# Kernel tuning notes

Hardware: AMD Instinct MI355X
Metric: run time of the kernel (lower is better)

Reference implementation:

```python
import jax, jax.numpy as jnp
import numpy as np

N = 50000   # nodes
E = 800000  # edges (avg degree 16)
D = 96      # in = hid = out
BN_EPS = 1e-5


def setup_inputs() -> dict:
    key = jax.random.key(0)
    ks = jax.random.split(key, 16)
    features = jax.random.normal(ks[0], (N, D), jnp.float32)
    src = jax.random.randint(ks[1], (E,), 0, N)
    dst = jax.random.randint(ks[2], (E,), 0, N)
    bound = 1.0 / np.sqrt(D)
    def lin(kw, kb):
        W = jax.random.uniform(kw, (D, D), jnp.float32, -bound, bound)
        b = jax.random.uniform(kb, (D,), jnp.float32, -bound, bound)
        return W, b
    W1, b1 = lin(ks[3], ks[4])
    W2, b2 = lin(ks[5], ks[6])
    W3, b3 = lin(ks[7], ks[8])
    gamma1 = jnp.ones((D,), jnp.float32)
    beta1 = jnp.zeros((D,), jnp.float32)
    gamma2 = jnp.ones((D,), jnp.float32)
    beta2 = jnp.zeros((D,), jnp.float32)
    return dict(features=features, W1=W1, b1=b1, gamma1=gamma1, beta1=beta1,
                W2=W2, b2=b2, gamma2=gamma2, beta2=beta2, W3=W3, b3=b3,
                src=src, dst=dst)


def _gin_conv(h, W, b, src, dst, inv_deg):
    # mean-aggregate incoming neighbor features, eps = 0: (h + mean_nb) @ W + b
    agg = jax.ops.segment_sum(h[src], dst, num_segments=N) * inv_deg[:, None]
    return (h + agg) @ W + b


def _batchnorm(x, gamma, beta):
    mu = jnp.mean(x, axis=0)
    var = jnp.mean((x - mu) ** 2, axis=0)  # biased, as torch BN training
    return (x - mu) * jax.lax.rsqrt(var + BN_EPS) * gamma + beta


def reference(features, W1, b1, gamma1, beta1, W2, b2, gamma2, beta2, W3, b3, src, dst):
    deg = jax.ops.segment_sum(jnp.ones((E,), jnp.float32), dst, num_segments=N)
    inv_deg = jnp.where(deg > 0, 1.0 / jnp.maximum(deg, 1.0), 0.0)
    h = _gin_conv(features, W1, b1, src, dst, inv_deg)
    h = jax.nn.relu(_batchnorm(h, gamma1, beta1))  # dropout p=0 -> identity
    h = _gin_conv(h, W2, b2, src, dst, inv_deg)
    h = jax.nn.relu(_batchnorm(h, gamma2, beta2))
    h = _gin_conv(h, W3, b3, src, dst, inv_deg)
    return h
```

## Files before the change

kernel.cpp:

```cpp
#include <hip/hip_runtime.h>

#define FD 96
#define NB12 12
#define BSH 7
#define BNODES 128
#define NBLK 256

typedef float  f32x4 __attribute__((ext_vector_type(4)));
typedef short  s16x8 __attribute__((ext_vector_type(8)));

__device__ __forceinline__ unsigned short f2bf(float x) {
    unsigned u = __float_as_uint(x);
    u = (u + 0x7fffu + ((u >> 16) & 1u)) >> 16;
    return (unsigned short)u;
}
__device__ __forceinline__ float bflo(unsigned u) { return __uint_as_float(u << 16); }
__device__ __forceinline__ float bfhi(unsigned u) { return __uint_as_float(u & 0xffff0000u); }


__global__ void k_bcount(const int* __restrict__ dst, int* __restrict__ bcnt, int E, int nbkt) {
    __shared__ int hist[512];
    int tid = threadIdx.x;
    if (tid < 512) hist[tid] = 0;
    __syncthreads();
    for (int i = blockIdx.x * blockDim.x + tid; i < E; i += gridDim.x * blockDim.x)
        atomicAdd(&hist[dst[i] >> BSH], 1);
    __syncthreads();
    if (tid < nbkt && hist[tid]) atomicAdd(&bcnt[tid], hist[tid]);
}

__global__ void k_bscan(const int* __restrict__ bcnt, int* __restrict__ bbase, int nbkt) {
    __shared__ int sh[512];
    int tid = threadIdx.x;
    int v = (tid < nbkt) ? bcnt[tid] : 0;
    sh[tid] = v;
    __syncthreads();
    for (int off = 1; off < 512; off <<= 1) {
        int t = (tid >= off) ? sh[tid - off] : 0;
        __syncthreads();
        sh[tid] += t;
        __syncthreads();
    }
    int incl = sh[tid];
    if (tid < nbkt) bbase[tid] = incl - v;
    if (tid == nbkt - 1) bbase[nbkt] = incl;
}

__global__ void k_h2d(const int* __restrict__ dst, int* __restrict__ hist2d,
                      int E, int nbkt, int chunk) {
    __shared__ int hist[512];
    int tid = threadIdx.x, b = blockIdx.x;
    for (int i = tid; i < 512; i += 256) hist[i] = 0;
    __syncthreads();
    int lo = b * chunk, hi = min(lo + chunk, E);
    for (int i = lo + tid; i < hi; i += 256)
        atomicAdd(&hist[dst[i] >> BSH], 1);
    __syncthreads();
    for (int q = tid; q < nbkt; q += 256)
        hist2d[(size_t)q * NBLK + b] = hist[q];
}

__global__ void k_cscan(const int* __restrict__ hist2d, const int* __restrict__ bbase,
                        int* __restrict__ cursor2d) {
    __shared__ int sh[NBLK];
    int q = blockIdx.x, tid = threadIdx.x;
    int v = hist2d[(size_t)q * NBLK + tid];
    sh[tid] = v;
    __syncthreads();
    for (int off = 1; off < NBLK; off <<= 1) {
        int t = (tid >= off) ? sh[tid - off] : 0;
        __syncthreads();
        sh[tid] += t;
        __syncthreads();
    }
    cursor2d[(size_t)q * NBLK + tid] = bbase[q] + sh[tid] - v;
}

__global__ void k_scat(const int* __restrict__ src, const int* __restrict__ dst,
                       const int* __restrict__ cursor2d, uint2* __restrict__ ebuf,
                       int E, int nbkt, int chunk) {
    __shared__ int cur[512];
    int tid = threadIdx.x, b = blockIdx.x;
    for (int q = tid; q < nbkt; q += 256)
        cur[q] = cursor2d[(size_t)q * NBLK + b];
    __syncthreads();
    int lo = b * chunk, hi = min(lo + chunk, E);
    for (int i = lo + tid; i < hi; i += 256) {
        int d = dst[i];
        int p = atomicAdd(&cur[d >> BSH], 1);
        ebuf[p] = make_uint2((unsigned)d, (unsigned)src[i]);
    }
}

__global__ void k_bsort(const uint2* __restrict__ ebuf, const int* __restrict__ bbase,
                        int* __restrict__ csr, int* __restrict__ rp, int* __restrict__ re,
                        float* __restrict__ invd, int n) {
    __shared__ int cnt[BNODES];
    __shared__ int cur[BNODES];
    const int b = blockIdx.x;
    const int tid = threadIdx.x;
    const int lo = bbase[b], hi = bbase[b + 1];
    if (tid < BNODES) cnt[tid] = 0;
    __syncthreads();
    for (int i = lo + tid; i < hi; i += blockDim.x)
        atomicAdd(&cnt[(int)ebuf[i].x - (b << BSH)], 1);
    __syncthreads();
    int v = (tid < BNODES) ? cnt[tid] : 0;
    for (int off = 1; off < BNODES; off <<= 1) {
        int t = (tid < BNODES && tid >= off) ? cnt[tid - off] : 0;
        __syncthreads();
        if (tid < BNODES) cnt[tid] += t;
        __syncthreads();
    }
    if (tid < BNODES) {
        int excl = cnt[tid] - v;
        int node = (b << BSH) + tid;
        if (node < n) {
            rp[node] = lo + excl;
            re[node] = lo + excl + v;
            invd[node] = (v > 0) ? (1.0f / (float)v) : 0.f;
        }
        cur[tid] = excl;
    }
    __syncthreads();
    for (int i = lo + tid; i < hi; i += blockDim.x) {
        uint2 e2 = ebuf[i];
        int local = (int)e2.x - (b << BSH);
        int p = lo + atomicAdd(&cur[local], 1);
        csr[p] = (int)e2.y;
    }
}


__global__ void k_cvt(const float4* __restrict__ in, uint4* __restrict__ o, int n16) {
    int i = blockIdx.x * blockDim.x + threadIdx.x;
    if (i >= n16) return;
    float4 x = in[2 * i], y = in[2 * i + 1];
    uint4 r;
    r.x = (unsigned)f2bf(x.x) | ((unsigned)f2bf(x.y) << 16);
    r.y = (unsigned)f2bf(x.z) | ((unsigned)f2bf(x.w) << 16);
    r.z = (unsigned)f2bf(y.x) | ((unsigned)f2bf(y.y) << 16);
    r.w = (unsigned)f2bf(y.z) | ((unsigned)f2bf(y.w) << 16);
    o[i] = r;
}


__global__ void k_wprep(const float* __restrict__ W, unsigned short* __restrict__ Wt) {
    int i = blockIdx.x * blockDim.x + threadIdx.x;
    if (i >= FD * FD) return;
    int col = i % FD, k = i / FD;
    Wt[col * FD + k] = f2bf(W[i]);
}


template<int NORM>
__global__ __launch_bounds__(256, 4) void k_agg(
    const uint4* __restrict__ h,
    const int* __restrict__ rp, const int* __restrict__ re,
    const int* __restrict__ csr, const float* __restrict__ invd,
    const float* __restrict__ nA, const float* __restrict__ nC,
    uint4* __restrict__ t, int n)
{
    int g = blockIdx.x * blockDim.x + threadIdx.x;
    int node = g / NB12;
    if (node >= n) return;
    int q = g - node * NB12;
    float a[8], c[8];
    if (NORM) {
        #pragma unroll
        for (int z = 0; z < 8; z++) { a[z] = nA[q * 8 + z]; c[z] = nC[q * 8 + z]; }
    }
    float acc8[8];
    #pragma unroll
    for (int z = 0; z < 8; z++) acc8[z] = 0.f;

    int e = rp[node];
    const int end = re[node];
    for (; e + 8 <= end; e += 8) {
        uint4 raw[8];
        #pragma unroll
        for (int u = 0; u < 8; u++) raw[u] = h[(size_t)csr[e + u] * NB12 + q];
        #pragma unroll
        for (int u = 0; u < 8; u++) {
            float v[8];
            v[0] = bflo(raw[u].x); v[1] = bfhi(raw[u].x);
            v[2] = bflo(raw[u].y); v[3] = bfhi(raw[u].y);
            v[4] = bflo(raw[u].z); v[5] = bfhi(raw[u].z);
            v[6] = bflo(raw[u].w); v[7] = bfhi(raw[u].w);
            #pragma unroll
            for (int z = 0; z < 8; z++) {
                float x = v[z];
                if (NORM) x = fmaxf(fmaf(a[z], x, c[z]), 0.f);
                acc8[z] += x;
            }
        }
    }
    for (; e < end; e++) {
        uint4 raw = h[(size_t)csr[e] * NB12 + q];
        float v[8];
        v[0] = bflo(raw.x); v[1] = bfhi(raw.x);
        v[2] = bflo(raw.y); v[3] = bfhi(raw.y);
        v[4] = bflo(raw.z); v[5] = bfhi(raw.z);
        v[6] = bflo(raw.w); v[7] = bfhi(raw.w);
        #pragma unroll
        for (int z = 0; z < 8; z++) {
            float x = v[z];
            if (NORM) x = fmaxf(fmaf(a[z], x, c[z]), 0.f);
            acc8[z] += x;
        }
    }
    uint4 rs = h[(size_t)node * NB12 + q];
    float xs[8];
    xs[0] = bflo(rs.x); xs[1] = bfhi(rs.x);
    xs[2] = bflo(rs.y); xs[3] = bfhi(rs.y);
    xs[4] = bflo(rs.z); xs[5] = bfhi(rs.z);
    xs[6] = bflo(rs.w); xs[7] = bfhi(rs.w);
    float id = invd[node];
    float o[8];
    #pragma unroll
    for (int z = 0; z < 8; z++) {
        float x = xs[z];
        if (NORM) x = fmaxf(fmaf(a[z], x, c[z]), 0.f);
        o[z] = fmaf(id, acc8[z], x);
    }
    uint4 pk;
    pk.x = (unsigned)f2bf(o[0]) | ((unsigned)f2bf(o[1]) << 16);
    pk.y = (unsigned)f2bf(o[2]) | ((unsigned)f2bf(o[3]) << 16);
    pk.z = (unsigned)f2bf(o[4]) | ((unsigned)f2bf(o[5]) << 16);
    pk.w = (unsigned)f2bf(o[6]) | ((unsigned)f2bf(o[7]) << 16);
    t[(size_t)node * NB12 + q] = pk;
}


template<int STATS, int OBF>
__global__ void k_mm(const unsigned short* __restrict__ ta,
                     const unsigned short* __restrict__ Wt,
                     const float* __restrict__ bias,
                     unsigned short* __restrict__ yb, float* __restrict__ yf,
                     float* __restrict__ accg, int n)
{
    __shared__ float sred[2 * FD];
    const int tid  = threadIdx.x;
    const int lane = tid & 63;
    const int wv   = tid >> 6;
    const int colb = lane & 15;
    const int hg   = lane >> 4;
    const int rbase = blockIdx.x * 64 + wv * 16;
    const int r = rbase + colb;

    s16x8 a[3];
    if (r < n) {
        #pragma unroll
        for (int s = 0; s < 3; s++)
            a[s] = *reinterpret_cast<const s16x8*>(ta + (size_t)r * FD + s * 32 + hg * 8);
    } else {
        #pragma unroll
        for (int s = 0; s < 3; s++) a[s] = s16x8{0, 0, 0, 0, 0, 0, 0, 0};
    }
    s16x8 b[6][3];
    #pragma unroll
    for (int c2 = 0; c2 < 6; c2++)
        #pragma unroll
        for (int s = 0; s < 3; s++)
            b[c2][s] = *reinterpret_cast<const s16x8*>(Wt + (size_t)(c2 * 16 + colb) * FD + s * 32 + hg * 8);

    f32x4 acc[6];
    #pragma unroll
    for (int c2 = 0; c2 < 6; c2++) acc[c2] = (f32x4){0.f, 0.f, 0.f, 0.f};
    #pragma unroll
    for (int s = 0; s < 3; s++)
        #pragma unroll
        for (int c2 = 0; c2 < 6; c2++)
            acc[c2] = __builtin_amdgcn_mfma_f32_16x16x32_bf16(a[s], b[c2][s], acc[c2], 0, 0, 0);

    float s1[6], s2[6];
    #pragma unroll
    for (int c2 = 0; c2 < 6; c2++) { s1[c2] = 0.f; s2[c2] = 0.f; }
    #pragma unroll
    for (int c2 = 0; c2 < 6; c2++) {
        float bc = bias[c2 * 16 + colb];
        #pragma unroll
        for (int j = 0; j < 4; j++) {
            int rr = rbase + hg * 4 + j;
            if (rr < n) {
                float y = acc[c2][j] + bc;
                if (OBF) yb[(size_t)rr * FD + c2 * 16 + colb] = f2bf(y);
                else     yf[(size_t)rr * FD + c2 * 16 + colb] = y;
                if (STATS) { s1[c2] += y; s2[c2] = fmaf(y, y, s2[c2]); }
            }
        }
    }
    if (STATS) {
        if (tid < 2 * FD) sred[tid] = 0.f;
        __syncthreads();
        #pragma unroll
        for (int c2 = 0; c2 < 6; c2++) {
            float v1 = s1[c2], v2 = s2[c2];
            v1 += __shfl_xor(v1, 16, 64); v1 += __shfl_xor(v1, 32, 64);
            v2 += __shfl_xor(v2, 16, 64); v2 += __shfl_xor(v2, 32, 64);
            if (lane < 16) {
                atomicAdd(&sred[c2 * 16 + colb], v1);
                atomicAdd(&sred[FD + c2 * 16 + colb], v2);
            }
        }
        __syncthreads();
        if (tid < 2 * FD) atomicAdd(&accg[tid], sred[tid]);
    }
}

__global__ void k_bnfin(const float* __restrict__ acc,
                        const float* __restrict__ gamma, const float* __restrict__ beta,
                        float* __restrict__ na, float* __restrict__ nc, float invN) {
    int f = threadIdx.x;
    float mu  = acc[f] * invN;
    float var = acc[FD + f] * invN - mu * mu;
    float a = gamma[f] * rsqrtf(var + 1e-5f);
    na[f] = a;
    nc[f] = beta[f] - mu * a;
}

extern "C" void kernel_launch(void* const* d_in, const int* in_sizes, int n_in,
                              void* d_out, int out_size, void* d_ws, size_t ws_size,
                              hipStream_t stream) {
    const float* feat = (const float*)d_in[0];
    const float* W1   = (const float*)d_in[1];
    const float* b1   = (const float*)d_in[2];
    const float* g1   = (const float*)d_in[3];
    const float* be1  = (const float*)d_in[4];
    const float* W2   = (const float*)d_in[5];
    const float* b2   = (const float*)d_in[6];
    const float* g2   = (const float*)d_in[7];
    const float* be2  = (const float*)d_in[8];
    const float* W3   = (const float*)d_in[9];
    const float* b3   = (const float*)d_in[10];
    const int*   src  = (const int*)d_in[11];
    const int*   dst  = (const int*)d_in[12];

    const int n = in_sizes[0] / FD;
    const int e = in_sizes[11];
    const int nbkt = (n + BNODES - 1) >> BSH;
    const int chunk = (e + NBLK - 1) / NBLK;

    char* w = (char*)d_ws;
    unsigned short* hf0 = (unsigned short*)w; w += (size_t)n * FD * 2;
    unsigned short* tb  = (unsigned short*)w; w += (size_t)n * FD * 2;
    unsigned short* Wt1 = (unsigned short*)w; w += FD * FD * 2;
    unsigned short* Wt2 = (unsigned short*)w; w += FD * FD * 2;
    unsigned short* Wt3 = (unsigned short*)w; w += FD * FD * 2;
    int*   csr     = (int*)w;   w += (size_t)e * 4;
    int*   bcnt    = (int*)w;   w += 512 * 4;
    float* acc1    = (float*)w; w += 2 * FD * 4;
    float* acc2    = (float*)w; w += 2 * FD * 4;
    int*   bbase   = (int*)w;   w += 513 * 4;
    int*   hist2d  = (int*)w;   w += (size_t)512 * NBLK * 4;
    int*   cursor2d= (int*)w;   w += (size_t)512 * NBLK * 4;
    int*   rp      = (int*)w;   w += (size_t)n * 4;
    int*   re      = (int*)w;   w += (size_t)n * 4;
    float* invd    = (float*)w; w += (size_t)n * 4;
    float* na1     = (float*)w; w += FD * 4;
    float* nc1     = (float*)w; w += FD * 4;
    float* na2     = (float*)w; w += FD * 4;
    float* nc2     = (float*)w; w += FD * 4;

    uint2* ebuf = (uint2*)tb;

    unsigned short* yb = (unsigned short*)d_out;
    float* O = (float*)d_out;
    const float invN = 1.0f / (float)n;
    const int AGG_GRID = (n * NB12 + 255) / 256;
    const int MM_GRID  = (n + 63) / 64;
    const int n16 = n * FD / 8;

    hipMemsetAsync(bcnt, 0, (512 + 4 * FD) * 4, stream);
    k_cvt<<<(n16 + 255) / 256, 256, 0, stream>>>((const float4*)feat, (uint4*)hf0, n16);
    k_wprep<<<(FD * FD + 255) / 256, 256, 0, stream>>>(W1, Wt1);
    k_wprep<<<(FD * FD + 255) / 256, 256, 0, stream>>>(W2, Wt2);
    k_wprep<<<(FD * FD + 255) / 256, 256, 0, stream>>>(W3, Wt3);

    k_bcount<<<128, 512, 0, stream>>>(dst, bcnt, e, nbkt);
    k_bscan<<<1, 512, 0, stream>>>(bcnt, bbase, nbkt);
    k_h2d<<<NBLK, 256, 0, stream>>>(dst, hist2d, e, nbkt, chunk);
    k_cscan<<<nbkt, NBLK, 0, stream>>>(hist2d, bbase, cursor2d);
    k_scat<<<NBLK, 256, 0, stream>>>(src, dst, cursor2d, ebuf, e, nbkt, chunk);
    k_bsort<<<nbkt, 256, 0, stream>>>(ebuf, bbase, csr, rp, re, invd, n);

    k_agg<0><<<AGG_GRID, 256, 0, stream>>>((const uint4*)hf0, rp, re, csr, invd,
                                           nullptr, nullptr, (uint4*)tb, n);
    k_mm<1, 1><<<MM_GRID, 256, 0, stream>>>(tb, Wt1, b1, yb, nullptr, acc1, n);
    k_bnfin<<<1, FD, 0, stream>>>(acc1, g1, be1, na1, nc1, invN);

    k_agg<1><<<AGG_GRID, 256, 0, stream>>>((const uint4*)yb, rp, re, csr, invd,
                                           na1, nc1, (uint4*)tb, n);
    k_mm<1, 1><<<MM_GRID, 256, 0, stream>>>(tb, Wt2, b2, yb, nullptr, acc2, n);
    k_bnfin<<<1, FD, 0, stream>>>(acc2, g2, be2, na2, nc2, invN);

    k_agg<1><<<AGG_GRID, 256, 0, stream>>>((const uint4*)yb, rp, re, csr, invd,
                                           na2, nc2, (uint4*)tb, n);
    k_mm<0, 0><<<MM_GRID, 256, 0, stream>>>(tb, Wt3, b3, nullptr, O, nullptr, n);
}
```

Measured before the change: 237.5 us.

## Degree-sort nodes within buckets for aggregation balance; fuse bucket count into h2d

k_bsort now builds a per-bucket permutation that groups the nodes of each 128-node bucket by in-degree (capped at 63) using a shared-memory counting sort. k_agg reads node ids through this permutation, so threads in a wavefront handle nodes of similar degree and idle less while waiting on long neighbour lists. The separate k_bcount pass is removed by having k_h2d atomically add its per-block histograms into the global bucket counts, saving one launch and one read of dst. The cost is an extra perm load per thread and scattered node order, which weakens the locality of the rp, re and output accesses in aggregation.

```diff
diff --git a/kernel.cpp b/kernel.cpp
--- a/kernel.cpp
+++ b/kernel.cpp
@@ -18,15 +18,21 @@
 __device__ __forceinline__ float bfhi(unsigned u) { return __uint_as_float(u & 0xffff0000u); }
 
 
-__global__ void k_bcount(const int* __restrict__ dst, int* __restrict__ bcnt, int E, int nbkt) {
+__global__ void k_h2d(const int* __restrict__ dst, int* __restrict__ hist2d,
+                      int* __restrict__ bcnt, int E, int nbkt, int chunk) {
     __shared__ int hist[512];
-    int tid = threadIdx.x;
-    if (tid < 512) hist[tid] = 0;
-    __syncthreads();
-    for (int i = blockIdx.x * blockDim.x + tid; i < E; i += gridDim.x * blockDim.x)
+    int tid = threadIdx.x, b = blockIdx.x;
+    for (int i = tid; i < 512; i += 256) hist[i] = 0;
+    __syncthreads();
+    int lo = b * chunk, hi = min(lo + chunk, E);
+    for (int i = lo + tid; i < hi; i += 256)
         atomicAdd(&hist[dst[i] >> BSH], 1);
     __syncthreads();
-    if (tid < nbkt && hist[tid]) atomicAdd(&bcnt[tid], hist[tid]);
+    for (int q = tid; q < nbkt; q += 256) {
+        int hv = hist[q];
+        hist2d[(size_t)q * NBLK + b] = hv;
+        if (hv) atomicAdd(&bcnt[q], hv);
+    }
 }
 
 __global__ void k_bscan(const int* __restrict__ bcnt, int* __restrict__ bbase, int nbkt) {
@@ -44,20 +50,6 @@
     int incl = sh[tid];
     if (tid < nbkt) bbase[tid] = incl - v;
     if (tid == nbkt - 1) bbase[nbkt] = incl;
-}
-
-__global__ void k_h2d(const int* __restrict__ dst, int* __restrict__ hist2d,
-                      int E, int nbkt, int chunk) {
-    __shared__ int hist[512];
-    int tid = threadIdx.x, b = blockIdx.x;
-    for (int i = tid; i < 512; i += 256) hist[i] = 0;
-    __syncthreads();
-    int lo = b * chunk, hi = min(lo + chunk, E);
-    for (int i = lo + tid; i < hi; i += 256)
-        atomicAdd(&hist[dst[i] >> BSH], 1);
-    __syncthreads();
-    for (int q = tid; q < nbkt; q += 256)
-        hist2d[(size_t)q * NBLK + b] = hist[q];
 }
 
 __global__ void k_cscan(const int* __restrict__ hist2d, const int* __restrict__ bbase,
@@ -94,31 +86,46 @@
 
 __global__ void k_bsort(const uint2* __restrict__ ebuf, const int* __restrict__ bbase,
                         int* __restrict__ csr, int* __restrict__ rp, int* __restrict__ re,
-                        float* __restrict__ invd, int n) {
+                        float* __restrict__ invd, int* __restrict__ perm, int n) {
     __shared__ int cnt[BNODES];
     __shared__ int cur[BNODES];
+    __shared__ int dh[64];
     const int b = blockIdx.x;
     const int tid = threadIdx.x;
     const int lo = bbase[b], hi = bbase[b + 1];
     if (tid < BNODES) cnt[tid] = 0;
+    if (tid < 64) dh[tid] = 0;
     __syncthreads();
     for (int i = lo + tid; i < hi; i += blockDim.x)
         atomicAdd(&cnt[(int)ebuf[i].x - (b << BSH)], 1);
     __syncthreads();
-    int v = (tid < BNODES) ? cnt[tid] : 0;
+    const int node = (b << BSH) + tid;
+    const int v = (tid < BNODES) ? cnt[tid] : 0;
+    const int dcl = min(v, 63);
+    if (tid < BNODES && node < n) atomicAdd(&dh[dcl], 1);
     for (int off = 1; off < BNODES; off <<= 1) {
         int t = (tid < BNODES && tid >= off) ? cnt[tid - off] : 0;
         __syncthreads();
         if (tid < BNODES) cnt[tid] += t;
         __syncthreads();
     }
+    int dv = (tid < 64) ? dh[tid] : 0;
+    for (int off = 1; off < 64; off <<= 1) {
+        int t = (tid < 64 && tid >= off) ? dh[tid - off] : 0;
+        __syncthreads();
+        if (tid < 64) dh[tid] += t;
+        __syncthreads();
+    }
+    if (tid < 64) dh[tid] -= dv;
+    __syncthreads();
     if (tid < BNODES) {
         int excl = cnt[tid] - v;
-        int node = (b << BSH) + tid;
         if (node < n) {
             rp[node] = lo + excl;
             re[node] = lo + excl + v;
             invd[node] = (v > 0) ? (1.0f / (float)v) : 0.f;
+            int r = atomicAdd(&dh[dcl], 1);
+            perm[(b << BSH) + r] = node;
         }
         cur[tid] = excl;
     }
@@ -158,13 +165,15 @@
     const uint4* __restrict__ h,
     const int* __restrict__ rp, const int* __restrict__ re,
     const int* __restrict__ csr, const float* __restrict__ invd,
+    const int* __restrict__ perm,
     const float* __restrict__ nA, const float* __restrict__ nC,
     uint4* __restrict__ t, int n)
 {
     int g = blockIdx.x * blockDim.x + threadIdx.x;
-    int node = g / NB12;
-    if (node >= n) return;
-    int q = g - node * NB12;
+    int idx = g / NB12;
+    if (idx >= n) return;
+    int node = perm[idx];
+    int q = g - idx * NB12;
     float a[8], c[8];
     if (NORM) {
         #pragma unroll
@@ -357,6 +366,7 @@
     int*   rp      = (int*)w;   w += (size_t)n * 4;
     int*   re      = (int*)w;   w += (size_t)n * 4;
     float* invd    = (float*)w; w += (size_t)n * 4;
+    int*   perm    = (int*)w;   w += (size_t)n * 4;
     float* na1     = (float*)w; w += FD * 4;
     float* nc1     = (float*)w; w += FD * 4;
     float* na2     = (float*)w; w += FD * 4;
@@ -377,24 +387,23 @@
     k_wprep<<<(FD * FD + 255) / 256, 256, 0, stream>>>(W2, Wt2);
     k_wprep<<<(FD * FD + 255) / 256, 256, 0, stream>>>(W3, Wt3);
 
-    k_bcount<<<128, 512, 0, stream>>>(dst, bcnt, e, nbkt);
+    k_h2d<<<NBLK, 256, 0, stream>>>(dst, hist2d, bcnt, e, nbkt, chunk);
     k_bscan<<<1, 512, 0, stream>>>(bcnt, bbase, nbkt);
-    k_h2d<<<NBLK, 256, 0, stream>>>(dst, hist2d, e, nbkt, chunk);
     k_cscan<<<nbkt, NBLK, 0, stream>>>(hist2d, bbase, cursor2d);
     k_scat<<<NBLK, 256, 0, stream>>>(src, dst, cursor2d, ebuf, e, nbkt, chunk);
-    k_bsort<<<nbkt, 256, 0, stream>>>(ebuf, bbase, csr, rp, re, invd, n);
-
-    k_agg<0><<<AGG_GRID, 256, 0, stream>>>((const uint4*)hf0, rp, re, csr, invd,
+    k_bsort<<<nbkt, 256, 0, stream>>>(ebuf, bbase, csr, rp, re, invd, perm, n);
+
+    k_agg<0><<<AGG_GRID, 256, 0, stream>>>((const uint4*)hf0, rp, re, csr, invd, perm,
                                            nullptr, nullptr, (uint4*)tb, n);
     k_mm<1, 1><<<MM_GRID, 256, 0, stream>>>(tb, Wt1, b1, yb, nullptr, acc1, n);
     k_bnfin<<<1, FD, 0, stream>>>(acc1, g1, be1, na1, nc1, invN);
 
-    k_agg<1><<<AGG_GRID, 256, 0, stream>>>((const uint4*)yb, rp, re, csr, invd,
+    k_agg<1><<<AGG_GRID, 256, 0, stream>>>((const uint4*)yb, rp, re, csr, invd, perm,
                                            na1, nc1, (uint4*)tb, n);
     k_mm<1, 1><<<MM_GRID, 256, 0, stream>>>(tb, Wt2, b2, yb, nullptr, acc2, n);
     k_bnfin<<<1, FD, 0, stream>>>(acc2, g2, be2, na2, nc2, invN);
 
-    k_agg<1><<<AGG_GRID, 256, 0, stream>>>((const uint4*)yb, rp, re, csr, invd,
+    k_agg<1><<<AGG_GRID, 256, 0, stream>>>((const uint4*)yb, rp, re, csr, invd, perm,
                                            na2, nc2, (uint4*)tb, n);
     k_mm<0, 0><<<MM_GRID, 256, 0, stream>>>(tb, Wt3, b3, nullptr, O, nullptr, n);
 }
```

Result: faster. 232.1 us (-2.3%).
